# Kernel optimization log

Hardware: AMD Instinct MI355X
Metric: run time of the kernel (lower is better)

Reference implementation:

```python
import jax, jax.numpy as jnp
import numpy as np

B, S, H, NH, DH, I, C, P = 4, 1024, 1280, 20, 64, 5120, 13, 8
LN_EPS = 1e-5


def setup_inputs() -> dict:
    key = jax.random.key(0)
    ks = jax.random.split(key, 20)
    n = lambda k, shp, s=0.02: (jax.random.normal(k, shp, jnp.float32) * s)
    return {
        "hidden_states": jax.random.normal(ks[0], (B, S, H), jnp.float32),
        "attention_mask": jnp.ones((B, S), jnp.float32),
        "Wq": n(ks[1], (H, H)), "bq": jnp.zeros((H,), jnp.float32),
        "Wk": n(ks[2], (H, H)), "bk": jnp.zeros((H,), jnp.float32),
        "Wv": n(ks[3], (H, H)), "bv": jnp.zeros((H,), jnp.float32),
        "W_ct1": n(ks[4], (P, C), 0.3), "b_ct1": jnp.zeros((P,), jnp.float32),
        "W_ct2": n(ks[5], (P, C), 0.3), "b_ct2": jnp.zeros((P,), jnp.float32),
        "M": n(ks[6], (C, C), 0.5),
        "bias_scale": jnp.full((1,), 0.5, jnp.float32),
        "W_ptm": n(ks[7], (P, H)), "b_ptm": jnp.zeros((P,), jnp.float32),
        "ln_g": jnp.ones((H,), jnp.float32), "ln_b": jnp.zeros((H,), jnp.float32),
        "Wf1": n(ks[8], (I, H)), "bf1": jnp.zeros((I,), jnp.float32),
        "Wf2": n(ks[9], (H, I)), "bf2": jnp.zeros((H,), jnp.float32),
    }


def reference(hidden_states, attention_mask, Wq, bq, Wk, bk, Wv, bv,
              W_ct1, b_ct1, W_ct2, b_ct2, M, bias_scale, W_ptm, b_ptm,
              ln_g, ln_b, Wf1, bf1, Wf2, bf2):
    h = hidden_states
    # crosstalk bilinear projection: (P,C) @ (C,P) -> (P,P)
    out1 = (M.T @ W_ct1.T + b_ct1).T          # (P, C)
    out2 = M @ W_ct2.T + b_ct2                # (C, P)
    R = out1 @ out2                           # (P, P)
    # ptm_predictor (Linear H->P) + softmax
    ptm = jax.nn.softmax(h @ W_ptm.T + b_ptm, axis=-1)            # (B,S,P)
    Bb = jnp.tanh(jnp.einsum('blc,cd,bmd->blm', ptm, R, ptm)) * bias_scale  # (B,S,S)
    # manual multi-head attention
    q = (h @ Wq.T + bq).reshape(B, S, NH, DH).transpose(0, 2, 1, 3)
    k = (h @ Wk.T + bk).reshape(B, S, NH, DH).transpose(0, 2, 1, 3)
    v = (h @ Wv.T + bv).reshape(B, S, NH, DH).transpose(0, 2, 1, 3)
    scores = jnp.einsum('bhld,bhmd->bhlm', q, k) / np.float32(np.sqrt(DH))
    scores = scores + Bb[:, None]
    scores = scores + (1.0 - attention_mask)[:, None, None, :] * jnp.finfo(h.dtype).min
    probs = jax.nn.softmax(scores, axis=-1)
    ctx = jnp.einsum('bhlm,bhmd->bhld', probs, v)
    ctx = ctx.transpose(0, 2, 1, 3).reshape(B, S, H)
    # residual + LayerNorm
    x = h + ctx
    mu = jnp.mean(x, -1, keepdims=True)
    var = jnp.var(x, -1, keepdims=True)
    x = (x - mu) * jax.lax.rsqrt(var + LN_EPS) * ln_g + ln_b
    # FFN with exact GELU, residual
    ff = jax.nn.gelu(x @ Wf1.T + bf1, approximate=False) @ Wf2.T + bf2
    return x + ff
```

## Files before the change

### kernel.cpp

```cpp
#include <hip/hip_runtime.h>
#include <math.h>

typedef _Float16 f16;
typedef _Float16 f16x2 __attribute__((ext_vector_type(2)));
typedef _Float16 f16x8 __attribute__((ext_vector_type(8)));
typedef _Float16 f16x4 __attribute__((ext_vector_type(4)));
typedef float f32x4 __attribute__((ext_vector_type(4)));

#define B_ 4
#define S_ 1024
#define H_ 1280
#define NH_ 20
#define DH_ 64
#define I_ 5120
#define C_ 13
#define P_ 8
#define LOG2E 1.44269504088896f

__device__ __forceinline__ void store_val(float* p, float v) { *p = v; }
__device__ __forceinline__ void store_val(f16* p, float v) { *p = (f16)v; }

__global__ __launch_bounds__(256) void cvt6_kernel(
    const float* __restrict__ s0, f16* __restrict__ d0, int n0,
    const float* __restrict__ s1, f16* __restrict__ d1, int n1,
    const float* __restrict__ s2, f16* __restrict__ d2, int n2,
    const float* __restrict__ s3, f16* __restrict__ d3, int n3,
    const float* __restrict__ s4, f16* __restrict__ d4, int n4,
    const float* __restrict__ s5, f16* __restrict__ d5, int n5) {
    int seg = blockIdx.y;
    const float* src = (seg == 0) ? s0 : (seg == 1) ? s1 : (seg == 2) ? s2
                     : (seg == 3) ? s3 : (seg == 4) ? s4 : s5;
    f16* dst = (seg == 0) ? d0 : (seg == 1) ? d1 : (seg == 2) ? d2
             : (seg == 3) ? d3 : (seg == 4) ? d4 : d5;
    int n = (seg == 0) ? n0 : (seg == 1) ? n1 : (seg == 2) ? n2
          : (seg == 3) ? n3 : (seg == 4) ? n4 : n5;
    int i = blockIdx.x * 256 + threadIdx.x;
    if (i < n) {
        f32x4 v = ((const f32x4*)src)[i];
        f16x4 o;
#pragma unroll
        for (int e = 0; e < 4; e++) o[e] = (f16)v[e];
        ((f16x4*)dst)[i] = o;
    }
}

__global__ __launch_bounds__(256) void ptm_kernel(const float* __restrict__ hin,
                                                  const float* __restrict__ Wptm,
                                                  const float* __restrict__ bptm,
                                                  const float* __restrict__ Mg,
                                                  const float* __restrict__ W1,
                                                  const float* __restrict__ b1,
                                                  const float* __restrict__ W2,
                                                  const float* __restrict__ b2,
                                                  float* __restrict__ ptm,
                                                  float* __restrict__ tg) {
    __shared__ float o1[P_][C_];
    __shared__ float o2[C_][P_];
    __shared__ float R[P_ * P_];
    int t = threadIdx.x;
    if (t < P_ * C_) {
        int p = t / C_, c = t % C_;
        float s = b1[p];
        for (int k = 0; k < C_; k++) s += Mg[k * C_ + c] * W1[p * C_ + k];
        o1[p][c] = s;
        int c2 = t / P_, p2 = t % P_;
        float s2 = b2[p2];
        for (int k = 0; k < C_; k++) s2 += Mg[c2 * C_ + k] * W2[p2 * C_ + k];
        o2[c2][p2] = s2;
    }
    __syncthreads();
    if (t < P_ * P_) {
        int p = t >> 3, q = t & 7;
        float s = 0.f;
        for (int c = 0; c < C_; c++) s += o1[p][c] * o2[c][q];
        R[t] = s;
    }
    __syncthreads();

    int wv = t >> 6, lane = t & 63;
    int row = blockIdx.x * 4 + wv;
    const float* hrow = hin + (size_t)row * H_;
    float acc[P_] = {};
    for (int i = 0; i < H_ / 64; i++) {
        int k = lane + 64 * i;
        float hv = hrow[k];
#pragma unroll
        for (int p = 0; p < P_; p++) acc[p] += hv * Wptm[p * H_ + k];
    }
#pragma unroll
    for (int p = 0; p < P_; p++) {
#pragma unroll
        for (int o = 32; o >= 1; o >>= 1) acc[p] += __shfl_xor(acc[p], o);
        acc[p] += bptm[p];
    }
    float mx = acc[0];
#pragma unroll
    for (int p = 1; p < P_; p++) mx = fmaxf(mx, acc[p]);
    float sum = 0.f;
#pragma unroll
    for (int p = 0; p < P_; p++) { acc[p] = expf(acc[p] - mx); sum += acc[p]; }
    float rinv = 1.f / sum;
#pragma unroll
    for (int p = 0; p < P_; p++) acc[p] *= rinv;
    float tv[P_];
#pragma unroll
    for (int d = 0; d < P_; d++) {
        float s = 0.f;
#pragma unroll
        for (int c = 0; c < P_; c++) s += acc[c] * R[c * P_ + d];
        tv[d] = s;
    }
    if (lane == 0) {
#pragma unroll
        for (int p = 0; p < P_; p++) {
            ptm[(size_t)row * P_ + p] = acc[p];
            tg[(size_t)row * P_ + p]  = tv[p];
        }
    }
}

__global__ __launch_bounds__(256) void bias_kernel(const float* __restrict__ tg,
                                                   const float* __restrict__ ptm,
                                                   const float* __restrict__ mask,
                                                   const float* __restrict__ bscale_p,
                                                   f16* __restrict__ bb) {
    const int bl = blockIdx.x;
    const int b = bl >> 10;
    const int t = threadIdx.x;
    __shared__ float tl[P_];
    if (t < P_) tl[t] = tg[(size_t)bl * P_ + t];
    __syncthreads();
    const float bscale = bscale_p[0];
    float t0 = tl[0], t1 = tl[1], t2 = tl[2], t3 = tl[3];
    float t4 = tl[4], t5 = tl[5], t6 = tl[6], t7 = tl[7];
#pragma unroll
    for (int i = 0; i < 4; i++) {
        int m = t + 256 * i;
        const float* pm = ptm + ((size_t)b * S_ + m) * P_;
        float4 p0 = *(const float4*)pm;
        float4 p1 = *(const float4*)(pm + 4);
        float d = t0 * p0.x + t1 * p0.y + t2 * p0.z + t3 * p0.w
                + t4 * p1.x + t5 * p1.y + t6 * p1.z + t7 * p1.w;
        float v = (tanhf(d) * bscale + (1.0f - mask[(size_t)b * S_ + m]) * (-30000.0f)) * LOG2E;
        bb[(size_t)bl * S_ + m] = (f16)v;
    }
}

template <int MODE, typename YT>
__device__ __forceinline__ void gemm_body(const f16* __restrict__ X,
                                          const f16* __restrict__ W,
                                          const float* __restrict__ bias,
                                          YT* __restrict__ Y,
                                          const f16* __restrict__ res,
                                          int Ndim, int Kdim, int kbeg, int kend,
                                          int m0, int n0, f16* sA, f16* sB) {
    const int t = threadIdx.x;
    const int lane = t & 63, w = t >> 6;
    const int wr = w >> 1, wc = w & 1;
    const int lr = lane & 15, kq = lane >> 4;

    f32x4 acc[4][4] = {};

    int s_row[4], s_gc[4];
#pragma unroll
    for (int inst = 0; inst < 4; inst++) {
        int ci = t + 256 * inst;
        s_row[inst] = ci >> 3;
        s_gc[inst] = (ci & 7) ^ (s_row[inst] & 7);
    }

    for (int k0 = kbeg; k0 < kend; k0 += 64) {
        __syncthreads();
#pragma unroll
        for (int inst = 0; inst < 4; inst++) {
            int ci = t + 256 * inst;
            __builtin_amdgcn_global_load_lds(
                (const unsigned*)(X + (size_t)(m0 + s_row[inst]) * Kdim + k0 + s_gc[inst] * 8),
                (unsigned*)(sA + ci * 8), 16, 0, 0);
        }
#pragma unroll
        for (int inst = 0; inst < 4; inst++) {
            int ci = t + 256 * inst;
            __builtin_amdgcn_global_load_lds(
                (const unsigned*)(W + (size_t)(n0 + s_row[inst]) * Kdim + k0 + s_gc[inst] * 8),
                (unsigned*)(sB + ci * 8), 16, 0, 0);
        }
        __syncthreads();
#pragma unroll
        for (int ks = 0; ks < 2; ks++) {
            f16x8 af[4], bf[4];
#pragma unroll
            for (int i = 0; i < 4; i++) {
                int row = wr * 64 + i * 16 + lr;
                int cl = (ks * 4 + kq) ^ (row & 7);
                af[i] = *(const f16x8*)(sA + row * 64 + cl * 8);
            }
#pragma unroll
            for (int j = 0; j < 4; j++) {
                int row = wc * 64 + j * 16 + lr;
                int cl = (ks * 4 + kq) ^ (row & 7);
                bf[j] = *(const f16x8*)(sB + row * 64 + cl * 8);
            }
#pragma unroll
            for (int i = 0; i < 4; i++)
#pragma unroll
                for (int j = 0; j < 4; j++)
                    acc[i][j] = __builtin_amdgcn_mfma_f32_16x16x32_f16(af[i], bf[j], acc[i][j], 0, 0, 0);
        }
    }
#pragma unroll
    for (int j = 0; j < 4; j++) {
        int col = n0 + wc * 64 + j * 16 + lr;
        float bcol = (MODE == 3) ? 0.f : bias[col];
#pragma unroll
        for (int i = 0; i < 4; i++) {
#pragma unroll
            for (int rr = 0; rr < 4; rr++) {
                int row = m0 + wr * 64 + i * 16 + kq * 4 + rr;
                float v = acc[i][j][rr] + bcol;
                if (MODE == 1) v = 0.5f * v * (1.0f + erff(v * 0.70710678118654752f));
                if (MODE == 2) v += (float)res[(size_t)row * Ndim + col];
                store_val(&Y[(size_t)row * Ndim + col], v);
            }
        }
    }
}

template <int MODE, typename YT>
__global__ __launch_bounds__(256, 2) void gemm128(const f16* __restrict__ X,
                                                  const f16* __restrict__ W,
                                                  const float* __restrict__ bias,
                                                  YT* __restrict__ Y,
                                                  const f16* __restrict__ res,
                                                  int Ndim, int Kdim) {
    __shared__ f16 sA[128 * 64];
    __shared__ f16 sB[128 * 64];
    gemm_body<MODE, YT>(X, W, bias, Y, res, Ndim, Kdim, 0, Kdim,
                        blockIdx.x * 128, blockIdx.y * 128, sA, sB);
}

__global__ __launch_bounds__(256, 2) void gemm_sk(const f16* __restrict__ X,
                                                  const f16* __restrict__ W,
                                                  float* __restrict__ Pb,
                                                  int Ndim, int Kdim, int Mdim) {
    __shared__ f16 sA[128 * 64];
    __shared__ f16 sB[128 * 64];
    const int kd2 = Kdim >> 1;
    float* Y = Pb + (size_t)blockIdx.z * Mdim * Ndim;
    gemm_body<3, float>(X, W, nullptr, Y, nullptr, Ndim, Kdim,
                        blockIdx.z * kd2, blockIdx.z * kd2 + kd2,
                        blockIdx.x * 128, blockIdx.y * 128, sA, sB);
}

__global__ __launch_bounds__(256) void reduce2_kernel(const float* __restrict__ p0,
                                                      const float* __restrict__ p1,
                                                      const float* __restrict__ bias,
                                                      const f16* __restrict__ res,
                                                      float* __restrict__ out) {
    int i = blockIdx.x * 256 + threadIdx.x;
    int col = (i * 4) % H_;
    f32x4 a = ((const f32x4*)p0)[i];
    f32x4 b = ((const f32x4*)p1)[i];
    f32x4 bc = *(const f32x4*)(bias + col);
    f16x4 r = ((const f16x4*)res)[i];
    f32x4 o;
#pragma unroll
    for (int e = 0; e < 4; e++) o[e] = a[e] + b[e] + bc[e] + (float)r[e];
    ((f32x4*)out)[i] = o;
}

__global__ __launch_bounds__(256, 2) void gemm_qkv(const f16* __restrict__ X,
                                                   const f16* __restrict__ Wq,
                                                   const f16* __restrict__ Wk,
                                                   const f16* __restrict__ Wv,
                                                   const float* __restrict__ bq,
                                                   const float* __restrict__ bk,
                                                   const float* __restrict__ bv,
                                                   f16* __restrict__ qb,
                                                   f16* __restrict__ kb,
                                                   f16* __restrict__ vb) {
    __shared__ f16 sA[128 * 64];
    __shared__ f16 sB[128 * 64];
    const int g = blockIdx.y / 10, nt = blockIdx.y % 10;
    const f16* W = (g == 0) ? Wq : (g == 1) ? Wk : Wv;
    const float* bias = (g == 0) ? bq : (g == 1) ? bk : bv;
    f16* Y = (g == 0) ? qb : (g == 1) ? kb : vb;
    gemm_body<0, f16>(X, W, bias, Y, nullptr, H_, H_, 0, H_,
                      blockIdx.x * 128, nt * 128, sA, sB);
}

__global__ __launch_bounds__(256) void attn_kernel(const f16* __restrict__ q,
                                                   const f16* __restrict__ k,
                                                   const f16* __restrict__ v,
                                                   const f16* __restrict__ bb,
                                                   const float* __restrict__ hin,
                                                   float* __restrict__ xpre) {
    __shared__ f16 sK[64 * 72];
    __shared__ f16 sVT[64 * 72];
    __shared__ f16 sP[64 * 72];

    const int t = threadIdx.x;
    const int w = t >> 6, lane = t & 63;
    const int lr = lane & 15, kq = lane >> 4;
    const int gid = blockIdx.x + 16 * (blockIdx.y + 20 * blockIdx.z);
    const int wk = (gid & 7) * 160 + (gid >> 3);
    const int l0 = (wk & 15) * 64;
    const int hb = wk >> 4;
    const int h = hb % 20, b = hb / 20;
    const size_t base = (size_t)b * S_ * H_ + (size_t)h * DH_;

    const int kr0 = t >> 3, kc8 = (t & 7) * 8;
    const int vr2 = (t >> 3) * 2, vc8 = (t & 7) * 8;
    const int vmsw = vr2 ^ vc8;
    const int br = t >> 2, bc16 = (t & 3) * 16;
    const f16* bbrow0 = bb + ((size_t)b * S_ + l0 + br) * S_;

    f16x8 kA0 = *(const f16x8*)&k[base + (size_t)kr0 * H_ + kc8];
    f16x8 kA1 = *(const f16x8*)&k[base + (size_t)(kr0 + 32) * H_ + kc8];
    f16x8 vA0 = *(const f16x8*)&v[base + (size_t)vr2 * H_ + vc8];
    f16x8 vA1 = *(const f16x8*)&v[base + (size_t)(vr2 + 1) * H_ + vc8];
    f16x8 bA0 = *(const f16x8*)(bbrow0 + bc16);
    f16x8 bA1 = *(const f16x8*)(bbrow0 + bc16 + 8);

    f16x8 afq[2];
#pragma unroll
    for (int ks = 0; ks < 2; ks++) {
        f16x8 qv = *(const f16x8*)&q[base + (size_t)(l0 + w * 16 + lr) * H_ + ks * 32 + kq * 8];
#pragma unroll
        for (int e = 0; e < 8; e++) qv[e] = (f16)((float)qv[e] * (0.125f * LOG2E));
        afq[ks] = qv;
    }

    f32x4 acc_o[4] = {};
    float lstate[4] = {};

    for (int mt = 0; mt < 16; mt++) {
        __syncthreads();
        *(f16x8*)&sK[kr0 * 72 + kc8] = kA0;
        *(f16x8*)&sK[(kr0 + 32) * 72 + kc8] = kA1;
#pragma unroll
        for (int e = 0; e < 8; e++) {
            f16x2 pk = {vA0[e], vA1[e]};
            *(f16x2*)&sVT[(vc8 + e) * 72 + vmsw] = pk;
        }
        *(f16x8*)&sP[br * 72 + bc16] = bA0;
        *(f16x8*)&sP[br * 72 + bc16 + 8] = bA1;
        const int m1 = ((mt + 1) & 15) * 64;
        f16x8 kB0 = *(const f16x8*)&k[base + (size_t)(m1 + kr0) * H_ + kc8];
        f16x8 kB1 = *(const f16x8*)&k[base + (size_t)(m1 + kr0 + 32) * H_ + kc8];
        f16x8 vB0 = *(const f16x8*)&v[base + (size_t)(m1 + vr2) * H_ + vc8];
        f16x8 vB1 = *(const f16x8*)&v[base + (size_t)(m1 + vr2 + 1) * H_ + vc8];
        f16x8 bB0 = *(const f16x8*)(bbrow0 + m1 + bc16);
        f16x8 bB1 = *(const f16x8*)(bbrow0 + m1 + bc16 + 8);
        __syncthreads();

        f32x4 sacc[4] = {};
        __builtin_amdgcn_s_setprio(1);
#pragma unroll
        for (int ks = 0; ks < 2; ks++)
#pragma unroll
            for (int j = 0; j < 4; j++) {
                f16x8 bk = *(const f16x8*)&sK[(j * 16 + lr) * 72 + ks * 32 + kq * 8];
                sacc[j] = __builtin_amdgcn_mfma_f32_16x16x32_f16(afq[ks], bk, sacc[j], 0, 0, 0);
            }
        __builtin_amdgcn_s_setprio(0);

#pragma unroll
        for (int j = 0; j < 4; j++)
#pragma unroll
            for (int rr = 0; rr < 4; rr++) {
                const int sp_addr = (w * 16 + kq * 4 + rr) * 72 + j * 16 + lr;
                float p = __builtin_exp2f(sacc[j][rr] + (float)sP[sp_addr]);
                lstate[rr] += p;
                sP[sp_addr] = (f16)p;
            }
        __syncthreads();

        f16x8 ap[2];
        ap[0] = *(const f16x8*)&sP[(w * 16 + lr) * 72 + kq * 8];
        ap[1] = *(const f16x8*)&sP[(w * 16 + lr) * 72 + 32 + kq * 8];
        __builtin_amdgcn_s_setprio(1);
#pragma unroll
        for (int ks = 0; ks < 2; ks++)
#pragma unroll
            for (int j2 = 0; j2 < 4; j2++) {
                int d = j2 * 16 + lr;
                int s_ = (d >> 3) & 7;
                f16x8 bv = *(const f16x8*)&sVT[d * 72 + 8 * (((ks << 2) + kq) ^ s_)];
                acc_o[j2] = __builtin_amdgcn_mfma_f32_16x16x32_f16(ap[ks], bv, acc_o[j2], 0, 0, 0);
            }
        __builtin_amdgcn_s_setprio(0);
        kA0 = kB0; kA1 = kB1; vA0 = vB0; vA1 = vB1; bA0 = bB0; bA1 = bB1;
    }

#pragma unroll
    for (int rr = 0; rr < 4; rr++) {
#pragma unroll
        for (int off = 8; off >= 1; off >>= 1) lstate[rr] += __shfl_xor(lstate[rr], off);
    }

#pragma unroll
    for (int rr = 0; rr < 4; rr++) {
        float linv = 1.0f / lstate[rr];
        int tok = l0 + w * 16 + kq * 4 + rr;
        size_t obase = base + (size_t)tok * H_;
#pragma unroll
        for (int j2 = 0; j2 < 4; j2++) {
            int d = j2 * 16 + lr;
            xpre[obase + d] = hin[obase + d] + acc_o[j2][rr] * linv;
        }
    }
}

__global__ __launch_bounds__(256) void ln_kernel(const float* __restrict__ xpre,
                                                 const float* __restrict__ g,
                                                 const float* __restrict__ bb,
                                                 f16* __restrict__ xln) {
    int row = blockIdx.x, t = threadIdx.x;
    const float* xr = xpre + (size_t)row * H_;
    float xv[5], s1 = 0.f, s2 = 0.f;
#pragma unroll
    for (int i = 0; i < 5; i++) {
        float v = xr[t + 256 * i];
        xv[i] = v; s1 += v; s2 += v * v;
    }
#pragma unroll
    for (int o = 32; o >= 1; o >>= 1) { s1 += __shfl_xor(s1, o); s2 += __shfl_xor(s2, o); }
    __shared__ float r1[4], r2[4];
    int wv = t >> 6, lane = t & 63;
    if (lane == 0) { r1[wv] = s1; r2[wv] = s2; }
    __syncthreads();
    float m1 = (r1[0] + r1[1] + r1[2] + r1[3]) * (1.0f / H_);
    float m2 = (r2[0] + r2[1] + r2[2] + r2[3]) * (1.0f / H_);
    float rstd = rsqrtf(m2 - m1 * m1 + 1e-5f);
#pragma unroll
    for (int i = 0; i < 5; i++) {
        int c = t + 256 * i;
        float v = (xv[i] - m1) * rstd * g[c] + bb[c];
        xln[(size_t)row * H_ + c] = (f16)v;
    }
}

extern "C" void kernel_launch(void* const* d_in, const int* in_sizes, int n_in,
                              void* d_out, int out_size, void* d_ws, size_t ws_size,
                              hipStream_t stream) {
    (void)in_sizes; (void)n_in; (void)out_size; (void)ws_size;
    const float* hin  = (const float*)d_in[0];
    const float* mask = (const float*)d_in[1];
    const float* Wq = (const float*)d_in[2];  const float* bq = (const float*)d_in[3];
    const float* Wk = (const float*)d_in[4];  const float* bk = (const float*)d_in[5];
    const float* Wv = (const float*)d_in[6];  const float* bv = (const float*)d_in[7];
    const float* Wct1 = (const float*)d_in[8];  const float* bct1 = (const float*)d_in[9];
    const float* Wct2 = (const float*)d_in[10]; const float* bct2 = (const float*)d_in[11];
    const float* Mg = (const float*)d_in[12];   const float* bscale = (const float*)d_in[13];
    const float* Wptm = (const float*)d_in[14]; const float* bptm = (const float*)d_in[15];
    const float* lng = (const float*)d_in[16];  const float* lnb = (const float*)d_in[17];
    const float* Wf1 = (const float*)d_in[18];  const float* bf1 = (const float*)d_in[19];
    const float* Wf2 = (const float*)d_in[20];  const float* bf2 = (const float*)d_in[21];

    char* ws = (char*)d_ws;
    const size_t SZ_PT  = (size_t)B_ * S_ * P_ * 4;
    const size_t SZ_H16 = (size_t)B_ * S_ * H_ * 2;
    const size_t SZ_H32 = (size_t)B_ * S_ * H_ * 4;
    const size_t SZ_WH  = (size_t)H_ * H_ * 2;
    const size_t SZ_WI  = (size_t)I_ * H_ * 2;
    float* ptm  = (float*)(ws + 256);
    float* tg   = (float*)(ws + 256 + SZ_PT);
    char* A0    = ws + 256 + 2 * SZ_PT;
    f16* hin16  = (f16*)(A0);
    f16* qb     = (f16*)(A0 + SZ_H16);
    f16* kb     = (f16*)(A0 + 2 * SZ_H16);
    f16* vb     = (f16*)(A0 + 3 * SZ_H16);
    float* xpre = (float*)(A0 + 4 * SZ_H16);
    f16* xln    = (f16*)(A0 + 4 * SZ_H16 + SZ_H32);
    f16* bbias  = (f16*)(A0 + 5 * SZ_H16 + SZ_H32);
    char* WA    = A0 + 5 * SZ_H16 + SZ_H32 + (size_t)B_ * S_ * S_ * 2;
    f16* Wq16   = (f16*)(WA);
    f16* Wk16   = (f16*)(WA + SZ_WH);
    f16* Wv16   = (f16*)(WA + 2 * SZ_WH);
    f16* Wf116  = (f16*)(WA + 3 * SZ_WH);
    f16* Wf216  = (f16*)(WA + 3 * SZ_WH + SZ_WI);
    f16* g1     = (f16*)(A0);
    float* pbuf = (float*)(WA + 3 * SZ_WH + 2 * SZ_WI);

    const int NH4 = (B_ * S_ * H_) / 4, NW4 = (H_ * H_) / 4, NI4 = (I_ * H_) / 4;
    cvt6_kernel<<<dim3((NI4 + 255) / 256, 6), 256, 0, stream>>>(
        hin, hin16, NH4, Wq, Wq16, NW4, Wk, Wk16, NW4,
        Wv, Wv16, NW4, Wf1, Wf116, NI4, Wf2, Wf216, NI4);

    ptm_kernel<<<S_ * B_ / 4, 256, 0, stream>>>(hin, Wptm, bptm,
                                                Mg, Wct1, bct1, Wct2, bct2, ptm, tg);
    bias_kernel<<<B_ * S_, 256, 0, stream>>>(tg, ptm, mask, bscale, bbias);
    gemm_qkv<<<dim3(32, 30), 256, 0, stream>>>(hin16, Wq16, Wk16, Wv16, bq, bk, bv, qb, kb, vb);
    attn_kernel<<<dim3(S_ / 64, NH_, B_), 256, 0, stream>>>(qb, kb, vb, bbias, hin, xpre);
    ln_kernel<<<B_ * S_, 256, 0, stream>>>(xpre, lng, lnb, xln);
    gemm128<1, f16><<<dim3(32, I_ / 128), 256, 0, stream>>>(xln, Wf116, bf1, g1, nullptr, I_, H_);
    gemm_sk<<<dim3(32, 10, 2), 256, 0, stream>>>(g1, Wf216, pbuf, H_, I_, B_ * S_);
    reduce2_kernel<<<(B_ * S_ * H_) / 4 / 256, 256, 0, stream>>>(
        pbuf, pbuf + (size_t)B_ * S_ * H_, bf2, xln, (float*)d_out);
}
```

Measured before the change: 452.8 us.

## Add 256x256 split-K FFN2 GEMM, fast GELU/tanh, fuse hin conversion

The FFN2 GEMM becomes a new 256x256-tile, 512-thread kernel with double-buffered direct global-to-LDS loads and 3-way split-K. The split-K partials are summed by a 3-input reduce that reuses xpre as the third buffer. GELU and tanh now use polynomial and exp2-based approximations instead of erff and tanhf. The f32-to-f16 conversion of hidden_states moves into the ptm kernel, and one __syncthreads is removed from the attention loop. The missing barrier could introduce a race on sP, and the approximations slightly change numerics.

```diff
diff --git a/kernel.cpp b/kernel.cpp
--- a/kernel.cpp
+++ b/kernel.cpp
@@ -20,20 +20,36 @@
 __device__ __forceinline__ void store_val(float* p, float v) { *p = v; }
 __device__ __forceinline__ void store_val(f16* p, float v) { *p = (f16)v; }
 
-__global__ __launch_bounds__(256) void cvt6_kernel(
+__device__ __forceinline__ float fast_gelu(float x) {
+    float ax = 0.70710678118654752f * fabsf(x);
+    float t = __builtin_amdgcn_rcpf(1.0f + 0.3275911f * ax);
+    float p = t * (0.254829592f + t * (-0.284496736f + t * (1.421413741f
+              + t * (-1.453152027f + t * 1.061405429f))));
+    float e = __builtin_exp2f(-(LOG2E) * ax * ax);
+    float er = 1.0f - p * e;
+    float cdf = 0.5f + 0.5f * (x >= 0.0f ? er : -er);
+    return x * cdf;
+}
+
+__device__ __forceinline__ float fast_tanh(float x) {
+    x = fminf(fmaxf(x, -20.0f), 20.0f);
+    float e = __builtin_exp2f(x * (2.0f * LOG2E));
+    return (e - 1.0f) * __builtin_amdgcn_rcpf(e + 1.0f);
+}
+
+__global__ __launch_bounds__(256) void cvt5_kernel(
     const float* __restrict__ s0, f16* __restrict__ d0, int n0,
     const float* __restrict__ s1, f16* __restrict__ d1, int n1,
     const float* __restrict__ s2, f16* __restrict__ d2, int n2,
     const float* __restrict__ s3, f16* __restrict__ d3, int n3,
-    const float* __restrict__ s4, f16* __restrict__ d4, int n4,
-    const float* __restrict__ s5, f16* __restrict__ d5, int n5) {
+    const float* __restrict__ s4, f16* __restrict__ d4, int n4) {
     int seg = blockIdx.y;
     const float* src = (seg == 0) ? s0 : (seg == 1) ? s1 : (seg == 2) ? s2
-                     : (seg == 3) ? s3 : (seg == 4) ? s4 : s5;
+                     : (seg == 3) ? s3 : s4;
     f16* dst = (seg == 0) ? d0 : (seg == 1) ? d1 : (seg == 2) ? d2
-             : (seg == 3) ? d3 : (seg == 4) ? d4 : d5;
+             : (seg == 3) ? d3 : d4;
     int n = (seg == 0) ? n0 : (seg == 1) ? n1 : (seg == 2) ? n2
-          : (seg == 3) ? n3 : (seg == 4) ? n4 : n5;
+          : (seg == 3) ? n3 : n4;
     int i = blockIdx.x * 256 + threadIdx.x;
     if (i < n) {
         f32x4 v = ((const f32x4*)src)[i];
@@ -53,7 +69,8 @@
                                                   const float* __restrict__ W2,
                                                   const float* __restrict__ b2,
                                                   float* __restrict__ ptm,
-                                                  float* __restrict__ tg) {
+                                                  float* __restrict__ tg,
+                                                  f16* __restrict__ hin16) {
     __shared__ float o1[P_][C_];
     __shared__ float o2[C_][P_];
     __shared__ float R[P_ * P_];
@@ -80,10 +97,12 @@
     int wv = t >> 6, lane = t & 63;
     int row = blockIdx.x * 4 + wv;
     const float* hrow = hin + (size_t)row * H_;
+    f16* hrow16 = hin16 + (size_t)row * H_;
     float acc[P_] = {};
     for (int i = 0; i < H_ / 64; i++) {
         int k = lane + 64 * i;
         float hv = hrow[k];
+        hrow16[k] = (f16)hv;
 #pragma unroll
         for (int p = 0; p < P_; p++) acc[p] += hv * Wptm[p * H_ + k];
     }
@@ -141,7 +160,7 @@
         float4 p1 = *(const float4*)(pm + 4);
         float d = t0 * p0.x + t1 * p0.y + t2 * p0.z + t3 * p0.w
                 + t4 * p1.x + t5 * p1.y + t6 * p1.z + t7 * p1.w;
-        float v = (tanhf(d) * bscale + (1.0f - mask[(size_t)b * S_ + m]) * (-30000.0f)) * LOG2E;
+        float v = (fast_tanh(d) * bscale + (1.0f - mask[(size_t)b * S_ + m]) * (-30000.0f)) * LOG2E;
         bb[(size_t)bl * S_ + m] = (f16)v;
     }
 }
@@ -218,8 +237,7 @@
             for (int rr = 0; rr < 4; rr++) {
                 int row = m0 + wr * 64 + i * 16 + kq * 4 + rr;
                 float v = acc[i][j][rr] + bcol;
-                if (MODE == 1) v = 0.5f * v * (1.0f + erff(v * 0.70710678118654752f));
-                if (MODE == 2) v += (float)res[(size_t)row * Ndim + col];
+                if (MODE == 1) v = fast_gelu(v);
                 store_val(&Y[(size_t)row * Ndim + col], v);
             }
         }
@@ -237,36 +255,6 @@
     __shared__ f16 sB[128 * 64];
     gemm_body<MODE, YT>(X, W, bias, Y, res, Ndim, Kdim, 0, Kdim,
                         blockIdx.x * 128, blockIdx.y * 128, sA, sB);
-}
-
-__global__ __launch_bounds__(256, 2) void gemm_sk(const f16* __restrict__ X,
-                                                  const f16* __restrict__ W,
-                                                  float* __restrict__ Pb,
-                                                  int Ndim, int Kdim, int Mdim) {
-    __shared__ f16 sA[128 * 64];
-    __shared__ f16 sB[128 * 64];
-    const int kd2 = Kdim >> 1;
-    float* Y = Pb + (size_t)blockIdx.z * Mdim * Ndim;
-    gemm_body<3, float>(X, W, nullptr, Y, nullptr, Ndim, Kdim,
-                        blockIdx.z * kd2, blockIdx.z * kd2 + kd2,
-                        blockIdx.x * 128, blockIdx.y * 128, sA, sB);
-}
-
-__global__ __launch_bounds__(256) void reduce2_kernel(const float* __restrict__ p0,
-                                                      const float* __restrict__ p1,
-                                                      const float* __restrict__ bias,
-                                                      const f16* __restrict__ res,
-                                                      float* __restrict__ out) {
-    int i = blockIdx.x * 256 + threadIdx.x;
-    int col = (i * 4) % H_;
-    f32x4 a = ((const f32x4*)p0)[i];
-    f32x4 b = ((const f32x4*)p1)[i];
-    f32x4 bc = *(const f32x4*)(bias + col);
-    f16x4 r = ((const f16x4*)res)[i];
-    f32x4 o;
-#pragma unroll
-    for (int e = 0; e < 4; e++) o[e] = a[e] + b[e] + bc[e] + (float)r[e];
-    ((f32x4*)out)[i] = o;
 }
 
 __global__ __launch_bounds__(256, 2) void gemm_qkv(const f16* __restrict__ X,
@@ -289,6 +277,182 @@
                       blockIdx.x * 128, nt * 128, sA, sB);
 }
 
+__global__ __launch_bounds__(512, 2) void gemm256_sk(const f16* __restrict__ X,
+                                                     const f16* __restrict__ W,
+                                                     float* __restrict__ p0,
+                                                     float* __restrict__ p1,
+                                                     float* __restrict__ p2,
+                                                     int Ndim, int Kdim) {
+    __shared__ f16 sA[2 * 16384];
+    __shared__ f16 sB[2 * 16384];
+    const int z = blockIdx.z;
+    float* __restrict__ Y = (z == 0) ? p0 : (z == 1) ? p1 : p2;
+    const int kbeg = z * 1728;
+    const int kend = (z == 2) ? Kdim : kbeg + 1728;
+    const int NT = (kend - kbeg) >> 6;
+    const int m0 = blockIdx.x * 256, n0 = blockIdx.y * 256;
+
+    const int t = threadIdx.x;
+    const int lane = t & 63, w = t >> 6;
+    const int wr = w >> 2, wc = w & 3;
+    const int lr = lane & 15, kq = lane >> 4;
+
+    const int rh0 = t >> 3;
+    const int gc0 = (t & 7) ^ (rh0 & 7);
+    const f16* Asrc = X + (size_t)(m0 + rh0) * Kdim + kbeg + gc0 * 8;
+    const f16* Bsrc = W + (size_t)(n0 + rh0) * Kdim + kbeg + gc0 * 8;
+
+    f32x4 acc[8][4] = {};
+
+#define STG_A(kt_) do { f16* d_ = sA + ((kt_) & 1) * 16384 + t * 8;            \
+        const f16* s_ = Asrc + (size_t)(kt_) * 64;                             \
+        __builtin_amdgcn_global_load_lds((const unsigned*)s_, (unsigned*)d_, 16, 0, 0); \
+        __builtin_amdgcn_global_load_lds((const unsigned*)(s_ + (size_t)64 * Kdim),  (unsigned*)(d_ + 4096), 16, 0, 0);  \
+        __builtin_amdgcn_global_load_lds((const unsigned*)(s_ + (size_t)128 * Kdim), (unsigned*)(d_ + 8192), 16, 0, 0);  \
+        __builtin_amdgcn_global_load_lds((const unsigned*)(s_ + (size_t)192 * Kdim), (unsigned*)(d_ + 12288), 16, 0, 0); \
+    } while (0)
+#define STG_B(kt_) do { f16* d_ = sB + ((kt_) & 1) * 16384 + t * 8;            \
+        const f16* s_ = Bsrc + (size_t)(kt_) * 64;                             \
+        __builtin_amdgcn_global_load_lds((const unsigned*)s_, (unsigned*)d_, 16, 0, 0); \
+        __builtin_amdgcn_global_load_lds((const unsigned*)(s_ + (size_t)64 * Kdim),  (unsigned*)(d_ + 4096), 16, 0, 0);  \
+        __builtin_amdgcn_global_load_lds((const unsigned*)(s_ + (size_t)128 * Kdim), (unsigned*)(d_ + 8192), 16, 0, 0);  \
+        __builtin_amdgcn_global_load_lds((const unsigned*)(s_ + (size_t)192 * Kdim), (unsigned*)(d_ + 12288), 16, 0, 0); \
+    } while (0)
+
+    STG_A(0); STG_B(0);
+    if (NT > 1) {
+        STG_A(1); STG_B(1);
+        asm volatile("s_waitcnt vmcnt(8)");
+    } else {
+        asm volatile("s_waitcnt vmcnt(0)");
+    }
+    __builtin_amdgcn_s_barrier();
+
+    for (int kt = 0; kt < NT; ++kt) {
+        const int p = kt & 1;
+        const f16* cA = sA + p * 16384;
+        const f16* cB = sB + p * 16384;
+        f16x8 a[4][2], b0[2][2], b1[2][2];
+
+#pragma unroll
+        for (int i = 0; i < 4; ++i) {
+            const int r = wr * 128 + (i + 4) * 16 + lr;
+#pragma unroll
+            for (int ks = 0; ks < 2; ++ks)
+                a[i][ks] = *(const f16x8*)(cA + r * 64 + (((ks * 4 + kq) ^ (r & 7)) * 8));
+        }
+#pragma unroll
+        for (int j = 0; j < 2; ++j) {
+            const int rb = wc * 64 + j * 16 + lr;
+#pragma unroll
+            for (int ks = 0; ks < 2; ++ks)
+                b0[j][ks] = *(const f16x8*)(cB + rb * 64 + (((ks * 4 + kq) ^ (rb & 7)) * 8));
+        }
+        __builtin_amdgcn_s_barrier();
+        __builtin_amdgcn_s_setprio(1);
+#pragma unroll
+        for (int ks = 0; ks < 2; ++ks)
+#pragma unroll
+            for (int i = 0; i < 4; ++i)
+#pragma unroll
+                for (int j = 0; j < 2; ++j)
+                    acc[i + 4][j] = __builtin_amdgcn_mfma_f32_16x16x32_f16(
+                        a[i][ks], b0[j][ks], acc[i + 4][j], 0, 0, 0);
+        __builtin_amdgcn_s_setprio(0);
+        __builtin_amdgcn_s_barrier();
+
+#pragma unroll
+        for (int j = 0; j < 2; ++j) {
+            const int rb = wc * 64 + (j + 2) * 16 + lr;
+#pragma unroll
+            for (int ks = 0; ks < 2; ++ks)
+                b1[j][ks] = *(const f16x8*)(cB + rb * 64 + (((ks * 4 + kq) ^ (rb & 7)) * 8));
+        }
+        __builtin_amdgcn_s_barrier();
+        __builtin_amdgcn_s_setprio(1);
+#pragma unroll
+        for (int ks = 0; ks < 2; ++ks)
+#pragma unroll
+            for (int i = 0; i < 4; ++i)
+#pragma unroll
+                for (int j = 0; j < 2; ++j)
+                    acc[i + 4][j + 2] = __builtin_amdgcn_mfma_f32_16x16x32_f16(
+                        a[i][ks], b1[j][ks], acc[i + 4][j + 2], 0, 0, 0);
+        __builtin_amdgcn_s_setprio(0);
+        __builtin_amdgcn_s_barrier();
+
+#pragma unroll
+        for (int i = 0; i < 4; ++i) {
+            const int r = wr * 128 + i * 16 + lr;
+#pragma unroll
+            for (int ks = 0; ks < 2; ++ks)
+                a[i][ks] = *(const f16x8*)(cA + r * 64 + (((ks * 4 + kq) ^ (r & 7)) * 8));
+        }
+        if (kt + 2 < NT) STG_B(kt + 2);
+        __builtin_amdgcn_s_barrier();
+        __builtin_amdgcn_s_setprio(1);
+#pragma unroll
+        for (int ks = 0; ks < 2; ++ks)
+#pragma unroll
+            for (int i = 0; i < 4; ++i)
+#pragma unroll
+                for (int j = 0; j < 2; ++j)
+                    acc[i][j] = __builtin_amdgcn_mfma_f32_16x16x32_f16(
+                        a[i][ks], b0[j][ks], acc[i][j], 0, 0, 0);
+        __builtin_amdgcn_s_setprio(0);
+        __builtin_amdgcn_s_barrier();
+
+        if (kt + 2 < NT) STG_A(kt + 2);
+        __builtin_amdgcn_s_setprio(1);
+#pragma unroll
+        for (int ks = 0; ks < 2; ++ks)
+#pragma unroll
+            for (int i = 0; i < 4; ++i)
+#pragma unroll
+                for (int j = 0; j < 2; ++j)
+                    acc[i][j + 2] = __builtin_amdgcn_mfma_f32_16x16x32_f16(
+                        a[i][ks], b1[j][ks], acc[i][j + 2], 0, 0, 0);
+        __builtin_amdgcn_s_setprio(0);
+        if (kt + 2 < NT) asm volatile("s_waitcnt vmcnt(8)");
+        else             asm volatile("s_waitcnt vmcnt(0)");
+        __builtin_amdgcn_s_barrier();
+    }
+#undef STG_A
+#undef STG_B
+
+#pragma unroll
+    for (int j = 0; j < 4; ++j) {
+        const int col = n0 + wc * 64 + j * 16 + lr;
+#pragma unroll
+        for (int i = 0; i < 8; ++i) {
+#pragma unroll
+            for (int rr = 0; rr < 4; ++rr) {
+                const int row = m0 + wr * 128 + i * 16 + kq * 4 + rr;
+                Y[(size_t)row * Ndim + col] = acc[i][j][rr];
+            }
+        }
+    }
+}
+
+__global__ __launch_bounds__(256) void reduce3_kernel(const float* __restrict__ p0,
+                                                      const float* __restrict__ p1,
+                                                      const float* __restrict__ p2,
+                                                      const float* __restrict__ bias,
+                                                      const f16* __restrict__ res,
+                                                      float* __restrict__ out) {
+    int i = blockIdx.x * 256 + threadIdx.x;
+    int col = (i * 4) % H_;
+    f32x4 a = ((const f32x4*)p0)[i];
+    f32x4 b = ((const f32x4*)p1)[i];
+    f32x4 c = ((const f32x4*)p2)[i];
+    f32x4 bc = *(const f32x4*)(bias + col);
+    f16x4 r = ((const f16x4*)res)[i];
+    f32x4 o;
+#pragma unroll
+    for (int e = 0; e < 4; e++) o[e] = a[e] + b[e] + c[e] + bc[e] + (float)r[e];
+    ((f32x4*)out)[i] = o;
+}
+
 __global__ __launch_bounds__(256) void attn_kernel(const f16* __restrict__ q,
                                                    const f16* __restrict__ k,
                                                    const f16* __restrict__ v,
@@ -374,7 +538,6 @@
                 lstate[rr] += p;
                 sP[sp_addr] = (f16)p;
             }
-        __syncthreads();
 
         f16x8 ap[2];
         ap[0] = *(const f16x8*)&sP[(w * 16 + lr) * 72 + kq * 8];
@@ -483,19 +646,20 @@
     f16* g1     = (f16*)(A0);
     float* pbuf = (float*)(WA + 3 * SZ_WH + 2 * SZ_WI);
 
-    const int NH4 = (B_ * S_ * H_) / 4, NW4 = (H_ * H_) / 4, NI4 = (I_ * H_) / 4;
-    cvt6_kernel<<<dim3((NI4 + 255) / 256, 6), 256, 0, stream>>>(
-        hin, hin16, NH4, Wq, Wq16, NW4, Wk, Wk16, NW4,
-        Wv, Wv16, NW4, Wf1, Wf116, NI4, Wf2, Wf216, NI4);
+    const int NW4 = (H_ * H_) / 4, NI4 = (I_ * H_) / 4;
+    cvt5_kernel<<<dim3((NI4 + 255) / 256, 5), 256, 0, stream>>>(
+        Wq, Wq16, NW4, Wk, Wk16, NW4, Wv, Wv16, NW4,
+        Wf1, Wf116, NI4, Wf2, Wf216, NI4);
 
     ptm_kernel<<<S_ * B_ / 4, 256, 0, stream>>>(hin, Wptm, bptm,
-                                                Mg, Wct1, bct1, Wct2, bct2, ptm, tg);
+                                                Mg, Wct1, bct1, Wct2, bct2, ptm, tg, hin16);
     bias_kernel<<<B_ * S_, 256, 0, stream>>>(tg, ptm, mask, bscale, bbias);
     gemm_qkv<<<dim3(32, 30), 256, 0, stream>>>(hin16, Wq16, Wk16, Wv16, bq, bk, bv, qb, kb, vb);
     attn_kernel<<<dim3(S_ / 64, NH_, B_), 256, 0, stream>>>(qb, kb, vb, bbias, hin, xpre);
     ln_kernel<<<B_ * S_, 256, 0, stream>>>(xpre, lng, lnb, xln);
     gemm128<1, f16><<<dim3(32, I_ / 128), 256, 0, stream>>>(xln, Wf116, bf1, g1, nullptr, I_, H_);
-    gemm_sk<<<dim3(32, 10, 2), 256, 0, stream>>>(g1, Wf216, pbuf, H_, I_, B_ * S_);
-    reduce2_kernel<<<(B_ * S_ * H_) / 4 / 256, 256, 0, stream>>>(
-        pbuf, pbuf + (size_t)B_ * S_ * H_, bf2, xln, (float*)d_out);
-}
+    gemm256_sk<<<dim3(16, H_ / 256, 3), 512, 0, stream>>>(
+        g1, Wf216, pbuf, pbuf + (size_t)B_ * S_ * H_, xpre, H_, I_);
+    reduce3_kernel<<<(B_ * S_ * H_) / 4 / 256, 256, 0, stream>>>(
+        pbuf, pbuf + (size_t)B_ * S_ * H_, xpre, bf2, xln, (float*)d_out);
+}
```

Measured after the change: 454.4 us. Within noise of the previous version (+0.4%).
